# Performance work log

Measured on AMD Instinct MI355X. Metric: run time of the kernel, lower is better.

The kernel has to match this reference:

```python
import jax, jax.numpy as jnp
import numpy as np

# Matcher cost weights (from __init__ defaults)
COST_CLASS, COST_BBOX, COST_GIOU, COST_MASK, COST_DICE = 2.0, 5.0, 2.0, 5.0, 5.0
EPS_DICE = 1e-5


def _cxcywh_to_xyxy(b):
    cx, cy, w, h = b[..., 0], b[..., 1], b[..., 2], b[..., 3]
    return jnp.stack([cx - 0.5 * w, cy - 0.5 * h, cx + 0.5 * w, cy + 0.5 * h], axis=-1)


def _generalized_box_iou(b1, b2):
    # b1: [N,4] xyxy, b2: [M,4] xyxy -> [N,M] pairwise GIoU
    area1 = (b1[:, 2] - b1[:, 0]) * (b1[:, 3] - b1[:, 1])  # [N]
    area2 = (b2[:, 2] - b2[:, 0]) * (b2[:, 3] - b2[:, 1])  # [M]
    lt = jnp.maximum(b1[:, None, :2], b2[None, :, :2])  # [N,M,2]
    rb = jnp.minimum(b1[:, None, 2:], b2[None, :, 2:])
    wh = jnp.clip(rb - lt, 0.0)
    inter = wh[..., 0] * wh[..., 1]
    union = area1[:, None] + area2[None, :] - inter
    iou = inter / union
    lt_e = jnp.minimum(b1[:, None, :2], b2[None, :, :2])
    rb_e = jnp.maximum(b1[:, None, 2:], b2[None, :, 2:])
    wh_e = jnp.clip(rb_e - lt_e, 0.0)
    area_e = wh_e[..., 0] * wh_e[..., 1]
    return iou - (area_e - union) / area_e


def setup_inputs() -> dict:
    key = jax.random.key(0)
    k1, k2, k3, k4, k5, k6 = jax.random.split(key, 6)
    B, Q, C, H, W = 4, 300, 81, 160, 160
    M, Hm, Wm = 400, 256, 256
    return {
        "pred_logits": jax.random.normal(k1, (B, Q, C), dtype=jnp.float32),
        "pred_boxes": jax.random.uniform(k2, (B, Q, 4), dtype=jnp.float32),
        "pred_masks": jax.random.normal(k3, (B, Q, H, W), dtype=jnp.float32),
        "tgt_boxes": jax.random.uniform(k4, (M, 4), dtype=jnp.float32),
        "tgt_masks": jax.random.uniform(k5, (M, Hm, Wm), dtype=jnp.float32),
        "tgt_ids": jax.random.randint(k6, (M,), 0, C, dtype=jnp.int64)
        if jax.config.jax_enable_x64 else jax.random.randint(k6, (M,), 0, C, dtype=jnp.int32),
    }


def reference(pred_logits, pred_boxes, pred_masks, tgt_boxes, tgt_masks, tgt_ids):
    B, Q = pred_logits.shape[:2]
    H, W = pred_masks.shape[-2:]
    P = H * W
    M = tgt_ids.shape[0]

    out_prob = jax.nn.softmax(pred_logits.reshape(B * Q, -1), axis=-1)  # [N,C]
    out_bbox = pred_boxes.reshape(B * Q, 4)                             # [N,4]
    mask_logits = pred_masks.reshape(B * Q, P)                          # [N,P]

    # bilinear resize of GT masks to prediction resolution (align_corners=False)
    tgt = jax.image.resize(tgt_masks, (M, H, W), method="bilinear").reshape(M, P)

    cost_class = -out_prob[:, tgt_ids]                                  # [N,M]
    cost_bbox = jnp.sum(jnp.abs(out_bbox[:, None, :] - tgt_boxes[None, :, :]), axis=-1)
    cost_giou = -_generalized_box_iou(_cxcywh_to_xyxy(out_bbox), _cxcywh_to_xyxy(tgt_boxes))

    # fused pairwise mean-BCE: -(log p @ t^T + log(1-p) @ (1-t)^T) / P
    log_p = jax.nn.log_sigmoid(mask_logits)
    log_1mp = jax.nn.log_sigmoid(-mask_logits)
    cost_mask = -(log_p @ tgt.T + log_1mp @ (1.0 - tgt).T) / P

    p = jax.nn.sigmoid(mask_logits)
    numerator = 2.0 * (p @ tgt.T)
    denominator = p.sum(-1)[:, None] + tgt.sum(-1)[None, :]
    cost_dice = 1.0 - (numerator + EPS_DICE) / (denominator + EPS_DICE)

    C = (COST_BBOX * cost_bbox + COST_GIOU * cost_giou + COST_CLASS * cost_class
         + COST_MASK * cost_mask + COST_DICE * cost_dice)
    return C.reshape(B, Q, M)
```

## Files before the change

### kernel.cpp

```cpp
#include <hip/hip_runtime.h>
#include <cstdint>

#define N_PRED 1200
#define M_TGT  400
#define KDIM   25600
#define NCLS   81
#define MPAD   448
#define KZN    13
#define NBLK   38
#define TSLICE 28672

typedef __attribute__((ext_vector_type(8)))  short bf16x8;
typedef __attribute__((ext_vector_type(4)))  float f32x4;
typedef unsigned char uchar;

__device__ __forceinline__ ushort f2bf(float f) {
  union { float f; uint32_t u; } v; v.f = f;
  uint32_t u = v.u + 0x7fffu + ((v.u >> 16) & 1u);
  return (ushort)(u >> 16);
}

__device__ __forceinline__ float bf2f(ushort s) {
  union { uint32_t u; float f; } v; v.u = ((uint32_t)s) << 16;
  return v.f;
}

__device__ __forceinline__ uint32_t pk_fp8(float a, float b, float c, float d) {
  uint32_t v = (uint32_t)__builtin_amdgcn_cvt_pk_fp8_f32(a, b, 0, false);
  v = (uint32_t)__builtin_amdgcn_cvt_pk_fp8_f32(c, d, (int)v, true);
  return v;
}

__device__ __forceinline__ void gll16(const void* g, void* l) {
  __builtin_amdgcn_global_load_lds(
      (const __attribute__((address_space(1))) void*)g,
      (__attribute__((address_space(3))) void*)l, 16, 0, 0);
}

__global__ __launch_bounds__(256) void resize2(const float* __restrict__ tm,
                                               uchar* __restrict__ T,
                                               float* __restrict__ tsum) {
  __shared__ float rows[16][256];
  __shared__ float vbuf[8][256];

  int m = blockIdx.x, yt = blockIdx.y;
  int y0 = yt * 8;
  int t = threadIdx.x;

  int jbase = (int)ceilf((y0 + 0.5f) * 1.6f - 2.1f);

  const float* base = tm + (size_t)m * 65536;
  {
    int r = t >> 4;
    int c0 = (t & 15) * 16;
    int jr = min(max(jbase + r, 0), 255);
    const float4* src = reinterpret_cast<const float4*>(base + jr * 256 + c0);
#pragma unroll
    for (int i = 0; i < 4; ++i)
      *reinterpret_cast<float4*>(&rows[r][c0 + i * 4]) = src[i];
  }
  __syncthreads();

#pragma unroll
  for (int yy = 0; yy < 8; ++yy) {
    int y = y0 + yy;
    float s = (y + 0.5f) * 1.6f - 0.5f;
    int j0 = (int)ceilf(s - 1.6f);
    float w[4]; float wsum = 0.f;
#pragma unroll
    for (int a = 0; a < 4; ++a) {
      int j = j0 + a;
      float wv = fmaxf(0.f, 1.f - fabsf((float)j - s) * 0.625f);
      if (j < 0 || j > 255) wv = 0.f;
      w[a] = wv; wsum += wv;
    }
    float winv = __builtin_amdgcn_rcpf(wsum);
    float acc = 0.f;
    int rbase = j0 - jbase;
#pragma unroll
    for (int a = 0; a < 4; ++a) acc += w[a] * rows[rbase + a][t];
    vbuf[yy][t] = acc * winv;
  }
  __syncthreads();

  float bsum = 0.f;
  if (t < 160) {
    int yy = t / 20, ch = t - yy * 20;
    float o[8];
#pragma unroll
    for (int j = 0; j < 8; ++j) {
      int x = ch * 8 + j;
      float sx = (x + 0.5f) * 1.6f - 0.5f;
      int jx0 = (int)ceilf(sx - 1.6f);
      float wsum = 0.f, h = 0.f;
#pragma unroll
      for (int b = 0; b < 4; ++b) {
        int jj = jx0 + b;
        float wv = fmaxf(0.f, 1.f - fabsf((float)jj - sx) * 0.625f);
        if (jj < 0 || jj > 255) wv = 0.f;
        wsum += wv;
        h += wv * vbuf[yy][min(max(jj, 0), 255)];
      }
      h *= __builtin_amdgcn_rcpf(wsum);
      o[j] = h; bsum += h;
    }
    int p0 = (y0 + yy) * 160 + ch * 8;
    int kt = p0 >> 6, kq = (p0 >> 3) & 7;
    size_t a = ((size_t)(kt * 8 + kq) * MPAD + m) * 8;
    uint2 pk;
    pk.x = pk_fp8(o[0], o[1], o[2], o[3]);
    pk.y = pk_fp8(o[4], o[5], o[6], o[7]);
    *reinterpret_cast<uint2*>(&T[a]) = pk;
  }
#pragma unroll
  for (int o2 = 32; o2 > 0; o2 >>= 1) bsum += __shfl_down(bsum, o2, 64);
  __shared__ float red[4];
  int wid = t >> 6;
  if ((t & 63) == 0) red[wid] = bsum;
  __syncthreads();
  if (t == 0) atomicAdd(&tsum[m], red[0] + red[1] + red[2] + red[3]);
}

__global__ void ones_init(uchar* __restrict__ T) {
  int i = blockIdx.x * 256 + threadIdx.x;
  if (i < 3200) {
    uint2 v; v.x = 0x38383838u; v.y = 0x38383838u;
    *reinterpret_cast<uint2*>(&T[((size_t)i * MPAD + 400) * 8]) = v;
  }
}

__global__ __launch_bounds__(512, 4) void gemm_mega(
    const float* __restrict__ pm, const uchar* __restrict__ Tg,
    ushort* __restrict__ part, float* __restrict__ SP) {
  __shared__ uchar buf[2][TSLICE];
  __shared__ uchar abuf[2][2][32 * 72];

  int orig = blockIdx.x;
  int xcd = orig & 7, base = orig >> 3;
  int wgid = (xcd < 6 ? xcd * 62 : 372 + (xcd - 6) * 61) + base;
  int kz = wgid / NBLK;
  int bn = wgid - kz * NBLK;
  int koff  = (kz < 5) ? (32 * kz) : (160 + 30 * (kz - 5));
  int steps = (kz < 5) ? 32 : 30;

  int t = threadIdx.x, lane = t & 63, w = t >> 6;
  int rg = w >> 2, cg = w & 3;
  int l15 = lane & 15, kq = lane >> 4;

  bool is_b = (t < 256);

  int arow = t >> 4, kc4 = t & 15;
  int rowA = bn * 32 + arow;
  int rowAc = min(rowA, N_PRED - 1);
  const float* apf = pm + (size_t)rowAc * KDIM + koff * 64 + kc4 * 4;
  int awoff = arow * 72 + kc4 * 4;

  const uchar* tsrc = Tg + (size_t)koff * TSLICE;
  int bbase = (kq * MPAD + cg * 112 + l15) * 8;
  int afbase = (rg * 16 + l15) * 72 + kq * 8;

  f32x4 z = {0.f, 0.f, 0.f, 0.f};
  f32x4 acc1[7], acc2[7];
#pragma unroll
  for (int j = 0; j < 7; ++j) { acc1[j] = z; acc2[j] = z; }
  float stx = 0.f;

  union fragu { uint2 u; long long l; };

#define WAITV(N) asm volatile("s_waitcnt vmcnt(" #N ")" ::: "memory")

#define STAGE_B(BI, ST)                                                        \
  do {                                                                         \
    const uchar* s_ = tsrc + (size_t)(ST) * TSLICE;                            \
    _Pragma("unroll")                                                          \
    for (int i_ = 0; i_ < 7; ++i_) {                                           \
      int c_ = w * 7 + i_;                                                     \
      gll16(s_ + c_ * 1024 + lane * 16, &buf[BI][c_ * 1024]);                  \
    }                                                                          \
  } while (0)

#define CONVERT(NI, V)                                                         \
  do {                                                                         \
    float xs_[4] = {V.x, V.y, V.z, V.w};                                       \
    float sg_[4];                                                              \
    _Pragma("unroll")                                                          \
    for (int q_ = 0; q_ < 4; ++q_) {                                           \
      float a_ = xs_[q_];                                                      \
      float e_ = __expf(-fabsf(a_));                                           \
      float o_ = 1.f + e_;                                                     \
      float i_ = __builtin_amdgcn_rcpf(o_);                                    \
      sg_[q_] = (a_ >= 0.f) ? i_ : e_ * i_;                                    \
      stx += fmaxf(a_, 0.f) + __logf(o_);                                      \
    }                                                                          \
    *reinterpret_cast<uint32_t*>(&abuf[NI][0][awoff]) =                        \
        pk_fp8(xs_[0], xs_[1], xs_[2], xs_[3]);                                \
    *reinterpret_cast<uint32_t*>(&abuf[NI][1][awoff]) =                        \
        pk_fp8(sg_[0], sg_[1], sg_[2], sg_[3]);                                \
  } while (0)

#define ITER(ACUR, S)                                                          \
  do {                                                                         \
    if (is_b) WAITV(0);               \
    if ((S) + 2 < steps) {             \
      float4 nv_ = *reinterpret_cast<const float4*>(apf + ((S) + 2) * 64);     \
      if (ACUR) fB = nv_; else fA = nv_;                                       \
    }                                                                          \
    __builtin_amdgcn_s_barrier();                                              \
    __builtin_amdgcn_sched_barrier(0);                                         \
    if ((S) + 1 < steps) {                                                     \
      if (is_b) STAGE_B(ACUR ^ 1, (S) + 1);                                    \
      if (ACUR) CONVERT(0, fA); else CONVERT(1, fB);                           \
    }                                                                          \
    _Pragma("unroll")                                                          \
    for (int h_ = 0; h_ < 2; ++h_) {                                           \
      fragu ax_, ap_;                                                          \
      ax_.u = *reinterpret_cast<const uint2*>(&abuf[ACUR][0][afbase + h_ * 32]); \
      ap_.u = *reinterpret_cast<const uint2*>(&abuf[ACUR][1][afbase + h_ * 32]); \
      __builtin_amdgcn_s_setprio(1);                                           \
      _Pragma("unroll")                                                        \
      for (int j_ = 0; j_ < 7; ++j_) {                                         \
        fragu bv_;                                                             \
        bv_.u = *reinterpret_cast<const uint2*>(                               \
            &buf[ACUR][bbase + h_ * 14336 + j_ * 128]);                        \
        acc1[j_] = __builtin_amdgcn_mfma_f32_16x16x32_fp8_fp8(ax_.l, bv_.l, acc1[j_], 0, 0, 0); \
        acc2[j_] = __builtin_amdgcn_mfma_f32_16x16x32_fp8_fp8(ap_.l, bv_.l, acc2[j_], 0, 0, 0); \
      }                                                                        \
      __builtin_amdgcn_s_setprio(0);                                           \
    }                                                                          \
    asm volatile("s_waitcnt lgkmcnt(0)" ::: "memory");                         \
  } while (0)

  float4 fA, fB;
  {
    float4 f0 = *reinterpret_cast<const float4*>(apf);
    fB = *reinterpret_cast<const float4*>(apf + 64);
    if (is_b) STAGE_B(0, 0);
    CONVERT(0, f0);
  }
  asm volatile("s_waitcnt lgkmcnt(0)" ::: "memory");

  for (int s = 0; s < steps; s += 2) {
    ITER(0, s);
    ITER(1, s + 1);
  }
#undef ITER
#undef CONVERT
#undef STAGE_B
#undef WAITV

  stx += __shfl_xor(stx, 1, 16); stx += __shfl_xor(stx, 2, 16);
  stx += __shfl_xor(stx, 4, 16); stx += __shfl_xor(stx, 8, 16);
  if ((t & 15) == 0 && rowA < N_PRED)
    atomicAdd(SP + rowA, stx);

  ushort* p1 = part;
  ushort* p2 = part + (size_t)KZN * 1200 * MPAD;
#pragma unroll
  for (int j = 0; j < 7; ++j)
#pragma unroll
    for (int rr = 0; rr < 4; ++rr) {
      int gn = bn * 32 + rg * 16 + kq * 4 + rr;
      if (gn < N_PRED) {
        int gm = cg * 112 + j * 16 + l15;
        size_t o = ((size_t)gn * KZN + kz) * MPAD + gm;
        p1[o] = f2bf(acc1[j][rr]);
        p2[o] = f2bf(acc2[j][rr]);
      }
    }
}

__global__ void sumprow(const ushort* __restrict__ part, float* __restrict__ sump) {
  int n = blockIdx.x * 256 + threadIdx.x;
  if (n < N_PRED) {
    const ushort* p2 = part + (size_t)KZN * 1200 * MPAD + (size_t)n * KZN * MPAD + 400;
    float s = 0.f;
#pragma unroll
    for (int kz = 0; kz < KZN; ++kz) s += bf2f(p2[kz * MPAD]);
    sump[n] = s;
  }
}

__global__ void probs_kernel(const float* __restrict__ logits, float* __restrict__ probs) {
  int n = blockIdx.x;
  int l = threadIdx.x;
  const float* row = logits + n * NCLS;
  float v0 = row[l];
  bool has2 = (l + 64) < NCLS;
  float v1 = has2 ? row[l + 64] : -3.4e38f;
  float mx = fmaxf(v0, v1);
#pragma unroll
  for (int o = 1; o < 64; o <<= 1) mx = fmaxf(mx, __shfl_xor(mx, o, 64));
  float e0 = expf(v0 - mx);
  float e1 = has2 ? expf(v1 - mx) : 0.f;
  float sm = e0 + e1;
#pragma unroll
  for (int o = 1; o < 64; o <<= 1) sm += __shfl_xor(sm, o, 64);
  float inv = 1.f / sm;
  probs[n * NCLS + l] = e0 * inv;
  if (has2) probs[n * NCLS + l + 64] = e1 * inv;
}

__global__ void combine2(const ushort* __restrict__ part,
                         const float* __restrict__ SP, const float* __restrict__ sump,
                         const float* __restrict__ tsum, const float* __restrict__ probs,
                         const float* __restrict__ pboxes, const float* __restrict__ tboxes,
                         const int* __restrict__ tids, float* __restrict__ out) {
  int idx = blockIdx.x * 256 + threadIdx.x;
  int n = idx / M_TGT;
  int m = idx - n * M_TGT;

  const ushort* p1 = part + (size_t)n * (KZN * MPAD) + m;
  const ushort* p2 = p1 + (size_t)KZN * 1200 * MPAD;
  float A1 = 0.f, A2 = 0.f;
#pragma unroll
  for (int kz = 0; kz < KZN; ++kz) {
    A1 += bf2f(p1[kz * MPAD]);
    A2 += bf2f(p2[kz * MPAD]);
  }
  float cm = (SP[n] - A1) * (1.0f / (float)KDIM);
  float cd = 1.f - (2.f * A2 + 1e-5f) / (sump[n] + tsum[m] + 1e-5f);
  float cc = -probs[n * NCLS + tids[m]];

  float4 pb = reinterpret_cast<const float4*>(pboxes)[n];
  float4 tb = reinterpret_cast<const float4*>(tboxes)[m];
  float l1 = fabsf(pb.x - tb.x) + fabsf(pb.y - tb.y) + fabsf(pb.z - tb.z) + fabsf(pb.w - tb.w);
  float px1 = pb.x - 0.5f * pb.z, py1 = pb.y - 0.5f * pb.w;
  float px2 = pb.x + 0.5f * pb.z, py2 = pb.y + 0.5f * pb.w;
  float tx1 = tb.x - 0.5f * tb.z, ty1 = tb.y - 0.5f * tb.w;
  float tx2 = tb.x + 0.5f * tb.z, ty2 = tb.y + 0.5f * tb.w;
  float a1 = (px2 - px1) * (py2 - py1);
  float a2 = (tx2 - tx1) * (ty2 - ty1);
  float iw = fmaxf(fminf(px2, tx2) - fmaxf(px1, tx1), 0.f);
  float ih = fmaxf(fminf(py2, ty2) - fmaxf(py1, ty1), 0.f);
  float inter = iw * ih;
  float uni = a1 + a2 - inter;
  float iou = inter / uni;
  float ew = fmaxf(fmaxf(px2, tx2) - fminf(px1, tx1), 0.f);
  float eh = fmaxf(fmaxf(py2, ty2) - fminf(py1, ty1), 0.f);
  float ae = ew * eh;
  float giou = iou - (ae - uni) / ae;

  out[idx] = 5.f * l1 + 2.f * (-giou) + 2.f * cc + 5.f * cm + 5.f * cd;
}


__device__ __forceinline__ float sigf(float x) {
  return 1.f / (1.f + __expf(-x));
}

__global__ void resize_lin(const float* __restrict__ tm, ushort* __restrict__ T,
                           float* __restrict__ tsum) {
  int m = blockIdx.x;
  int p = blockIdx.y * 256 + threadIdx.x;
  int y = p / 160;
  int x = p - y * 160;
  float wy[4], wx[4];
  int jy0, jx0;
  {
    float s = (y + 0.5f) * 1.6f - 0.5f;
    jy0 = (int)ceilf(s - 1.6f);
    float ws = 0.f;
#pragma unroll
    for (int a = 0; a < 4; ++a) {
      int j = jy0 + a;
      float w = fmaxf(0.f, 1.f - fabsf((float)j - s) * 0.625f);
      if (j < 0 || j > 255) w = 0.f;
      wy[a] = w; ws += w;
    }
    float inv = 1.f / ws;
#pragma unroll
    for (int a = 0; a < 4; ++a) wy[a] *= inv;
  }
  {
    float s = (x + 0.5f) * 1.6f - 0.5f;
    jx0 = (int)ceilf(s - 1.6f);
    float ws = 0.f;
#pragma unroll
    for (int b = 0; b < 4; ++b) {
      int j = jx0 + b;
      float w = fmaxf(0.f, 1.f - fabsf((float)j - s) * 0.625f);
      if (j < 0 || j > 255) w = 0.f;
      wx[b] = w; ws += w;
    }
    float inv = 1.f / ws;
#pragma unroll
    for (int b = 0; b < 4; ++b) wx[b] *= inv;
  }
  const float* base = tm + (size_t)m * 65536;
  float acc = 0.f;
#pragma unroll
  for (int a = 0; a < 4; ++a) {
    int jy = min(max(jy0 + a, 0), 255);
    float wya = wy[a];
#pragma unroll
    for (int b = 0; b < 4; ++b) {
      int jx = min(max(jx0 + b, 0), 255);
      acc += wya * wx[b] * base[jy * 256 + jx];
    }
  }
  T[(size_t)m * KDIM + p] = f2bf(acc);
  float v = acc;
#pragma unroll
  for (int o = 32; o > 0; o >>= 1) v += __shfl_down(v, o, 64);
  __shared__ float red[4];
  int wid = threadIdx.x >> 6;
  if ((threadIdx.x & 63) == 0) red[wid] = v;
  __syncthreads();
  if (threadIdx.x == 0) atomicAdd(&tsum[m], red[0] + red[1] + red[2] + red[3]);
}

__global__ void stats_kernel(const float* __restrict__ pm, float* __restrict__ S,
                             float* __restrict__ sump) {
  int n = blockIdx.x;
  const float4* row = reinterpret_cast<const float4*>(pm + (size_t)n * KDIM);
  float ssp = 0.f, sp = 0.f;
  for (int i = threadIdx.x; i < KDIM / 4; i += 256) {
    float4 v = row[i];
    float xs[4] = {v.x, v.y, v.z, v.w};
#pragma unroll
    for (int j = 0; j < 4; ++j) {
      float x = xs[j];
      float e = __expf(-fabsf(x));
      float inv1pe = 1.f / (1.f + e);
      sp += (x >= 0.f) ? inv1pe : e * inv1pe;
      ssp += fmaxf(x, 0.f) + log1pf(e);
    }
  }
#pragma unroll
  for (int o = 32; o > 0; o >>= 1) {
    ssp += __shfl_down(ssp, o, 64);
    sp  += __shfl_down(sp, o, 64);
  }
  __shared__ float red[8];
  int wid = threadIdx.x >> 6;
  if ((threadIdx.x & 63) == 0) { red[wid] = ssp; red[4 + wid] = sp; }
  __syncthreads();
  if (threadIdx.x == 0) {
    S[n]    = -(red[0] + red[1] + red[2] + red[3]);
    sump[n] = red[4] + red[5] + red[6] + red[7];
  }
}

__device__ __forceinline__ bf16x8 load_frag_lin(const ushort* p) {
  union { ushort4 u[2]; bf16x8 f; } fr;
  fr.u[0] = *reinterpret_cast<const ushort4*>(p);
  fr.u[1] = *reinterpret_cast<const ushort4*>(p + 4);
  return fr.f;
}

__global__ __launch_bounds__(256) void gemm_fused(
    const float* __restrict__ pm, const ushort* __restrict__ T,
    ushort* __restrict__ part1, ushort* __restrict__ part2, int k_per) {
  __shared__ ushort Ax[64][40];
  __shared__ ushort Ap[64][40];
  __shared__ ushort Bs[64][40];
  int n0 = blockIdx.x * 64;
  int m0 = blockIdx.y * 64;
  int kz = blockIdx.z;
  int k_begin = kz * k_per;
  int t = threadIdx.x;
  int r = t >> 2;
  int q = t & 3;
  bool a_ok = (n0 + r) < N_PRED;
  bool b_ok = (m0 + r) < M_TGT;
  const float*  pA = pm + (size_t)(n0 + r) * KDIM + k_begin + q * 8;
  const ushort* pB = T  + (size_t)(m0 + r) * KDIM + k_begin + q * 8;
  int lane = t & 63;
  int w = t >> 6;
  int wr = (w >> 1) * 32;
  int wc = (w & 1) * 32;
  int lrow = lane & 15;
  int kc = (lane >> 4) * 8;
  f32x4 zero = {0.f, 0.f, 0.f, 0.f};
  f32x4 acc1[2][2] = {{zero, zero}, {zero, zero}};
  f32x4 acc2[2][2] = {{zero, zero}, {zero, zero}};
  int steps = k_per / 32;
  for (int kt = 0; kt < steps; ++kt) {
    __syncthreads();
    float4 f0 = {0.f,0.f,0.f,0.f}, f1 = {0.f,0.f,0.f,0.f};
    if (a_ok) {
      f0 = *reinterpret_cast<const float4*>(pA);
      f1 = *reinterpret_cast<const float4*>(pA + 4);
    }
    pA += 32;
    ushort4 xa, xb, pa, pb4;
    xa.x = f2bf(f0.x); xa.y = f2bf(f0.y); xa.z = f2bf(f0.z); xa.w = f2bf(f0.w);
    xb.x = f2bf(f1.x); xb.y = f2bf(f1.y); xb.z = f2bf(f1.z); xb.w = f2bf(f1.w);
    pa.x = f2bf(sigf(f0.x)); pa.y = f2bf(sigf(f0.y)); pa.z = f2bf(sigf(f0.z)); pa.w = f2bf(sigf(f0.w));
    pb4.x = f2bf(sigf(f1.x)); pb4.y = f2bf(sigf(f1.y)); pb4.z = f2bf(sigf(f1.z)); pb4.w = f2bf(sigf(f1.w));
    *reinterpret_cast<ushort4*>(&Ax[r][q * 8])     = xa;
    *reinterpret_cast<ushort4*>(&Ax[r][q * 8 + 4]) = xb;
    *reinterpret_cast<ushort4*>(&Ap[r][q * 8])     = pa;
    *reinterpret_cast<ushort4*>(&Ap[r][q * 8 + 4]) = pb4;
    union { uint4 u; ushort4 s[2]; } bv;
    bv.u = make_uint4(0, 0, 0, 0);
    if (b_ok) bv.u = *reinterpret_cast<const uint4*>(pB);
    pB += 32;
    *reinterpret_cast<ushort4*>(&Bs[r][q * 8])     = bv.s[0];
    *reinterpret_cast<ushort4*>(&Bs[r][q * 8 + 4]) = bv.s[1];
    __syncthreads();
    bf16x8 ax[2], ap[2], bb[2];
#pragma unroll
    for (int i = 0; i < 2; ++i) {
      ax[i] = load_frag_lin(&Ax[wr + i * 16 + lrow][kc]);
      ap[i] = load_frag_lin(&Ap[wr + i * 16 + lrow][kc]);
      bb[i] = load_frag_lin(&Bs[wc + i * 16 + lrow][kc]);
    }
#pragma unroll
    for (int i = 0; i < 2; ++i)
#pragma unroll
      for (int j = 0; j < 2; ++j) {
        acc1[i][j] = __builtin_amdgcn_mfma_f32_16x16x32_bf16(ax[i], bb[j], acc1[i][j], 0, 0, 0);
        acc2[i][j] = __builtin_amdgcn_mfma_f32_16x16x32_bf16(ap[i], bb[j], acc2[i][j], 0, 0, 0);
      }
  }
  int rowb = (lane >> 4) * 4;
  int col = lane & 15;
#pragma unroll
  for (int i = 0; i < 2; ++i)
#pragma unroll
    for (int j = 0; j < 2; ++j)
#pragma unroll
      for (int rr = 0; rr < 4; ++rr) {
        int gn = n0 + wr + i * 16 + rowb + rr;
        int gm = m0 + wc + j * 16 + col;
        if (gn < N_PRED && gm < M_TGT) {
          size_t o = (size_t)kz * 480000 + (size_t)gn * 400 + gm;
          part1[o] = f2bf(acc1[i][j][rr]);
          part2[o] = f2bf(acc2[i][j][rr]);
        }
      }
}

__global__ void combine_fb(const ushort* __restrict__ part1, const ushort* __restrict__ part2,
                           const float* __restrict__ S, const float* __restrict__ sump,
                           const float* __restrict__ tsum, const float* __restrict__ probs,
                           const float* __restrict__ pboxes, const float* __restrict__ tboxes,
                           const int* __restrict__ tids, float* __restrict__ out, int KZ) {
  int idx = blockIdx.x * 256 + threadIdx.x;
  int n = idx / M_TGT;
  int m = idx - n * M_TGT;
  float A1 = 0.f, A2 = 0.f;
  for (int kz = 0; kz < KZ; ++kz) {
    A1 += bf2f(part1[(size_t)kz * 480000 + idx]);
    A2 += bf2f(part2[(size_t)kz * 480000 + idx]);
  }
  float cm = -(A1 + S[n]) * (1.0f / (float)KDIM);
  float cd = 1.f - (2.f * A2 + 1e-5f) / (sump[n] + tsum[m] + 1e-5f);
  float cc = -probs[n * NCLS + tids[m]];
  float4 pb = reinterpret_cast<const float4*>(pboxes)[n];
  float4 tb = reinterpret_cast<const float4*>(tboxes)[m];
  float l1 = fabsf(pb.x - tb.x) + fabsf(pb.y - tb.y) + fabsf(pb.z - tb.z) + fabsf(pb.w - tb.w);
  float px1 = pb.x - 0.5f * pb.z, py1 = pb.y - 0.5f * pb.w;
  float px2 = pb.x + 0.5f * pb.z, py2 = pb.y + 0.5f * pb.w;
  float tx1 = tb.x - 0.5f * tb.z, ty1 = tb.y - 0.5f * tb.w;
  float tx2 = tb.x + 0.5f * tb.z, ty2 = tb.y + 0.5f * tb.w;
  float a1 = (px2 - px1) * (py2 - py1);
  float a2 = (tx2 - tx1) * (ty2 - ty1);
  float iw = fmaxf(fminf(px2, tx2) - fmaxf(px1, tx1), 0.f);
  float ih = fmaxf(fminf(py2, ty2) - fmaxf(py1, ty1), 0.f);
  float inter = iw * ih;
  float uni = a1 + a2 - inter;
  float iou = inter / uni;
  float ew = fmaxf(fmaxf(px2, tx2) - fminf(px1, tx1), 0.f);
  float eh = fmaxf(fmaxf(py2, ty2) - fminf(py1, ty1), 0.f);
  float ae = ew * eh;
  float giou = iou - (ae - uni) / ae;
  out[idx] = 5.f * l1 + 2.f * (-giou) + 2.f * cc + 5.f * cm + 5.f * cd;
}


extern "C" void kernel_launch(void* const* d_in, const int* in_sizes, int n_in,
                              void* d_out, int out_size, void* d_ws, size_t ws_size,
                              hipStream_t stream) {
  const float* logits = (const float*)d_in[0];
  const float* pboxes = (const float*)d_in[1];
  const float* pmasks = (const float*)d_in[2];
  const float* tboxes = (const float*)d_in[3];
  const float* tmasks = (const float*)d_in[4];
  const int*   tids   = (const int*)d_in[5];
  float* out = (float*)d_out;
  char* ws = (char*)d_ws;

  const size_t offT     = 0;
  const size_t offPart  = 24371200;
  const size_t offProbs = offPart + 27955200;
  const size_t offStats = offProbs + 390400;
  const size_t needNew  = offStats + 11200;

  if (ws_size >= needNew) {
    uchar* Tg    = (uchar*)(ws + offT);
    ushort* part = (ushort*)(ws + offPart);
    float* probs = (float*)(ws + offProbs);
    float* SP    = (float*)(ws + offStats);
    float* sump  = (float*)(ws + offStats + 4800);
    float* tsum  = (float*)(ws + offStats + 9600);

    hipMemsetAsync(SP, 0, 11200, stream);
    resize2<<<dim3(M_TGT, 20), 256, 0, stream>>>(tmasks, Tg, tsum);
    ones_init<<<13, 256, 0, stream>>>(Tg);
    probs_kernel<<<N_PRED, 64, 0, stream>>>(logits, probs);
    gemm_mega<<<NBLK * KZN, 512, 0, stream>>>(pmasks, Tg, part, SP);
    sumprow<<<5, 256, 0, stream>>>(part, sump);
    combine2<<<1875, 256, 0, stream>>>(part, SP, sump, tsum, probs,
                                       pboxes, tboxes, tids, out);
  } else {
    ushort* T     = (ushort*)ws;
    float*  probs = (float*)(ws + 20480000);
    float*  S     = (float*)(ws + 20868800);
    float*  sump  = (float*)(ws + 20873600);
    float*  tsum  = (float*)(ws + 20878400);
    ushort* part1 = (ushort*)(ws + 20880000);
    size_t need8 = 20880000ull + 2ull * 8 * 480000 * 2;
    int KZf = (ws_size >= need8) ? 8 : 1;
    ushort* part2 = part1 + (size_t)KZf * 480000;

    hipMemsetAsync(tsum, 0, M_TGT * sizeof(float), stream);
    resize_lin<<<dim3(M_TGT, 100), 256, 0, stream>>>(tmasks, T, tsum);
    probs_kernel<<<N_PRED, 64, 0, stream>>>(logits, probs);
    stats_kernel<<<N_PRED, 256, 0, stream>>>(pmasks, S, sump);
    gemm_fused<<<dim3(19, 7, KZf), 256, 0, stream>>>(pmasks, T, part1, part2, KDIM / KZf);
    combine_fb<<<1875, 256, 0, stream>>>(part1, part2, S, sump, tsum, probs,
                                         pboxes, tboxes, tids, out, KZf);
  }
}
```

Measured before the change: 133.8 us.

## Interleave fp8 K-chunks so LDS fragment reads use 16-byte loads

Changes the global target-mask layout and the shared-memory A-operand layout so that two 8-byte K chunks sit next to each other. Each lane can then fetch both MFMA fragments with one 128-bit LDS read instead of two 64-bit reads. The resize-producer, the ones-init kernel and the GEMM indexing are all updated together. The A buffer also loses its padding (72 to 64 bytes per row), which could bring LDS bank conflicts back.

```diff
diff --git a/kernel.cpp b/kernel.cpp
--- a/kernel.cpp
+++ b/kernel.cpp
@@ -105,8 +105,9 @@
       o[j] = h; bsum += h;
     }
     int p0 = (y0 + yy) * 160 + ch * 8;
-    int kt = p0 >> 6, kq = (p0 >> 3) & 7;
-    size_t a = ((size_t)(kt * 8 + kq) * MPAD + m) * 8;
+    int kt = p0 >> 6, kql = (p0 >> 3) & 7;
+    size_t a = (size_t)kt * TSLICE +
+               ((size_t)((kql & 3) * MPAD + m)) * 16 + (kql >> 2) * 8;
     uint2 pk;
     pk.x = pk_fp8(o[0], o[1], o[2], o[3]);
     pk.y = pk_fp8(o[4], o[5], o[6], o[7]);
@@ -124,8 +125,11 @@
 __global__ void ones_init(uchar* __restrict__ T) {
   int i = blockIdx.x * 256 + threadIdx.x;
   if (i < 3200) {
+    int kt = i >> 3, kql = i & 7;
+    size_t a = (size_t)kt * TSLICE +
+               ((size_t)((kql & 3) * MPAD + 400)) * 16 + (kql >> 2) * 8;
     uint2 v; v.x = 0x38383838u; v.y = 0x38383838u;
-    *reinterpret_cast<uint2*>(&T[((size_t)i * MPAD + 400) * 8]) = v;
+    *reinterpret_cast<uint2*>(&T[a]) = v;
   }
 }
 
@@ -133,7 +137,7 @@
     const float* __restrict__ pm, const uchar* __restrict__ Tg,
     ushort* __restrict__ part, float* __restrict__ SP) {
   __shared__ uchar buf[2][TSLICE];
-  __shared__ uchar abuf[2][2][32 * 72];
+  __shared__ uchar abuf[2][2][2048];
 
   int orig = blockIdx.x;
   int xcd = orig & 7, base = orig >> 3;
@@ -153,11 +157,12 @@
   int rowA = bn * 32 + arow;
   int rowAc = min(rowA, N_PRED - 1);
   const float* apf = pm + (size_t)rowAc * KDIM + koff * 64 + kc4 * 4;
-  int awoff = arow * 72 + kc4 * 4;
+  int kqlw = kc4 >> 1;
+  int awoff = ((kqlw & 3) * 32 + arow) * 16 + (kqlw >> 2) * 8 + (kc4 & 1) * 4;
 
   const uchar* tsrc = Tg + (size_t)koff * TSLICE;
-  int bbase = (kq * MPAD + cg * 112 + l15) * 8;
-  int afbase = (rg * 16 + l15) * 72 + kq * 8;
+  int bbase = (kq * MPAD + cg * 112 + l15) * 16;
+  int afoff = (kq * 32 + rg * 16 + l15) * 16;
 
   f32x4 z = {0.f, 0.f, 0.f, 0.f};
   f32x4 acc1[7], acc2[7];
@@ -165,7 +170,7 @@
   for (int j = 0; j < 7; ++j) { acc1[j] = z; acc2[j] = z; }
   float stx = 0.f;
 
-  union fragu { uint2 u; long long l; };
+  union fragu4 { uint4 u; long long l[2]; };
 
 #define WAITV(N) asm volatile("s_waitcnt vmcnt(" #N ")" ::: "memory")
 
@@ -200,7 +205,7 @@
 
 #define ITER(ACUR, S)                                                          \
   do {                                                                         \
-    if (is_b) WAITV(0);               \
+    if (is_b) WAITV(0);                   \
     if ((S) + 2 < steps) {             \
       float4 nv_ = *reinterpret_cast<const float4*>(apf + ((S) + 2) * 64);     \
       if (ACUR) fB = nv_; else fA = nv_;                                       \
@@ -211,19 +216,19 @@
       if (is_b) STAGE_B(ACUR ^ 1, (S) + 1);                                    \
       if (ACUR) CONVERT(0, fA); else CONVERT(1, fB);                           \
     }                                                                          \
-    _Pragma("unroll")                                                          \
-    for (int h_ = 0; h_ < 2; ++h_) {                                           \
-      fragu ax_, ap_;                                                          \
-      ax_.u = *reinterpret_cast<const uint2*>(&abuf[ACUR][0][afbase + h_ * 32]); \
-      ap_.u = *reinterpret_cast<const uint2*>(&abuf[ACUR][1][afbase + h_ * 32]); \
+    {                                                                          \
+      fragu4 ax_, ap_;                                                         \
+      ax_.u = *reinterpret_cast<const uint4*>(&abuf[ACUR][0][afoff]);          \
+      ap_.u = *reinterpret_cast<const uint4*>(&abuf[ACUR][1][afoff]);          \
       __builtin_amdgcn_s_setprio(1);                                           \
       _Pragma("unroll")                                                        \
       for (int j_ = 0; j_ < 7; ++j_) {                                         \
-        fragu bv_;                                                             \
-        bv_.u = *reinterpret_cast<const uint2*>(                               \
-            &buf[ACUR][bbase + h_ * 14336 + j_ * 128]);                        \
-        acc1[j_] = __builtin_amdgcn_mfma_f32_16x16x32_fp8_fp8(ax_.l, bv_.l, acc1[j_], 0, 0, 0); \
-        acc2[j_] = __builtin_amdgcn_mfma_f32_16x16x32_fp8_fp8(ap_.l, bv_.l, acc2[j_], 0, 0, 0); \
+        fragu4 bv_;                                                            \
+        bv_.u = *reinterpret_cast<const uint4*>(&buf[ACUR][bbase + j_ * 256]); \
+        acc1[j_] = __builtin_amdgcn_mfma_f32_16x16x32_fp8_fp8(ax_.l[0], bv_.l[0], acc1[j_], 0, 0, 0); \
+        acc2[j_] = __builtin_amdgcn_mfma_f32_16x16x32_fp8_fp8(ap_.l[0], bv_.l[0], acc2[j_], 0, 0, 0); \
+        acc1[j_] = __builtin_amdgcn_mfma_f32_16x16x32_fp8_fp8(ax_.l[1], bv_.l[1], acc1[j_], 0, 0, 0); \
+        acc2[j_] = __builtin_amdgcn_mfma_f32_16x16x32_fp8_fp8(ap_.l[1], bv_.l[1], acc2[j_], 0, 0, 0); \
       }                                                                        \
       __builtin_amdgcn_s_setprio(0);                                           \
     }                                                                          \
```

After: 128.4 us. -4.0%, faster.
